# Kernel optimization log

Hardware: AMD Instinct MI355X
Metric: run time of the kernel (lower is better)

Reference implementation:

```python
import jax, jax.numpy as jnp
import numpy as np

N_HEAD = 12
NEG_INF = -1e30


def setup_inputs() -> dict:
    key = jax.random.key(0)
    ks = jax.random.split(key, 12)
    bs, q_len, c_len, d = 2, 2048, 2048, 768
    s = 1.0 / np.sqrt(d)
    return {
        "query": jax.random.normal(ks[0], (bs, q_len, d), jnp.float32),
        "context": jax.random.normal(ks[1], (bs, c_len, d), jnp.float32),
        "c_mask": jax.random.randint(ks[2], (bs, c_len), 0, 2, jnp.int32),
        "Wq_w": jax.random.normal(ks[3], (d, d), jnp.float32) * s,
        "Wq_b": jnp.zeros((d,), jnp.float32),
        "Wk_w": jax.random.normal(ks[4], (d, d), jnp.float32) * s,
        "Wk_b": jnp.zeros((d,), jnp.float32),
        "Wv_w": jax.random.normal(ks[5], (d, d), jnp.float32) * s,
        "Wv_b": jnp.zeros((d,), jnp.float32),
        "fc_w": jax.random.normal(ks[6], (d, d), jnp.float32) * s,
        "fc_b": jnp.zeros((d,), jnp.float32),
    }


def reference(query, context, c_mask, Wq_w, Wq_b, Wk_w, Wk_b, Wv_w, Wv_b, fc_w, fc_b):
    bs, q_len, d = query.shape
    c_len = context.shape[1]
    d_k = d // N_HEAD
    a = 1.0 / np.sqrt(d_k)

    # QKV projections (torch Linear: y = x @ W.T + b), split into heads
    q = (query @ Wq_w.T + Wq_b).reshape(bs, q_len, N_HEAD, d_k)
    k = (context @ Wk_w.T + Wk_b).reshape(bs, c_len, N_HEAD, d_k)
    v = (context @ Wv_w.T + Wv_b).reshape(bs, c_len, N_HEAD, d_k)

    # scores [bs, n_head, q_len, c_len]
    s = jnp.einsum('bqhd,bchd->bhqc', q, k) * a

    # mask_logits: s * m + (1 - m) * -1e30, mask broadcast over heads and q
    m = c_mask.astype(s.dtype)[:, None, None, :]
    s = s * m + (1.0 - m) * NEG_INF

    p = jax.nn.softmax(s, axis=-1)  # dropout p=0.0 -> identity

    out = jnp.einsum('bhqc,bchd->bqhd', p, v).reshape(bs, q_len, d)
    return out @ fc_w.T + fc_b
```

## Files before the change

kernel.cpp:

```cpp
#include <hip/hip_runtime.h>
#include <cstdint>

#define D_MODEL 768
#define NH      12
#define DKH     64
#define SEQ     2048
#define BS      2
#define MROWS   (BS*SEQ)

typedef __bf16 bf16x8 __attribute__((ext_vector_type(8)));
typedef float  f32x4  __attribute__((ext_vector_type(4)));
typedef unsigned int u32_as1 __attribute__((address_space(1)));
typedef unsigned int u32_as3 __attribute__((address_space(3)));

__device__ __forceinline__ void gld16(const void* g, void* l) {
  __builtin_amdgcn_global_load_lds((const u32_as1*)g, (u32_as3*)l, 16, 0, 0);
}
__device__ __forceinline__ unsigned short f2bf(float x) {
  return __builtin_bit_cast(unsigned short, (__bf16)x);
}

__global__ void cvt_all(
    const float* __restrict__ q, const float* __restrict__ c,
    const float* __restrict__ wq, const float* __restrict__ wk,
    const float* __restrict__ wv, const float* __restrict__ wf,
    unsigned short* __restrict__ oq, unsigned short* __restrict__ oc,
    unsigned short* __restrict__ owq, unsigned short* __restrict__ owk,
    unsigned short* __restrict__ owv, unsigned short* __restrict__ owf)
{
  const int b = blockIdx.x;
  const float* in; unsigned short* out; int i;
  if (b < 6144) {
    in = (b < 3072) ? q : c;
    out = (b < 3072) ? oq : oc;
    i = ((b < 3072) ? b : b - 3072) * 256 + threadIdx.x;
  } else {
    int wb = b - 6144, wi = wb / 576;
    in  = (wi == 0) ? wq : (wi == 1) ? wk : (wi == 2) ? wv : wf;
    out = (wi == 0) ? owq : (wi == 1) ? owk : (wi == 2) ? owv : owf;
    i = (wb - wi * 576) * 256 + threadIdx.x;
  }
  float4 v = reinterpret_cast<const float4*>(in)[i];
  ushort4 o; o.x = f2bf(v.x); o.y = f2bf(v.y); o.z = f2bf(v.z); o.w = f2bf(v.w);
  reinterpret_cast<ushort4*>(out)[i] = o;
}

__global__ void mask_bf(const int* __restrict__ m, unsigned short* __restrict__ o) {
  int i = blockIdx.x * 256 + threadIdx.x;
  o[i] = f2bf(m[i] ? 1.0f : 0.0f);
}

template<bool OUT_F32>
__device__ __forceinline__ void gemm64x128_body(
    const unsigned short* __restrict__ A, const unsigned short* __restrict__ B,
    const float* __restrict__ bias, int biasRow, void* __restrict__ Cout,
    int ldc, int m0, int n0, float outScale, const int* __restrict__ colMask)
{
  __shared__ alignas(16) char sA[2][8192];
  __shared__ alignas(16) char sB[2][16384];
  const int tid = threadIdx.x;
  const int w = tid >> 6, l = tid & 63;
  const int g16 = l >> 4, c16 = l & 15;
  const int wr = (w >> 1) * 32, wc = (w & 1) * 64;

  auto stageA = [&](int kt, char* dst) {
#pragma unroll
    for (int i = 0; i < 2; i++) {
      int ch = w * 2 + i;
      int X = ch * 1024 + l * 16;
      int row = X >> 7;
      int sl = ((X >> 4) & 7) ^ (row & 7);
      gld16(A + (size_t)(m0 + row) * 768 + kt + sl * 8, dst + ch * 1024);
    }
  };
  auto stageB = [&](int kt, char* dst) {
#pragma unroll
    for (int i = 0; i < 4; i++) {
      int ch = w * 4 + i;
      int X = ch * 1024 + l * 16;
      int row = X >> 7;
      int sl = ((X >> 4) & 7) ^ (row & 7);
      gld16(B + (size_t)(n0 + row) * 768 + kt + sl * 8, dst + ch * 1024);
    }
  };

  f32x4 acc[2][4];
#pragma unroll
  for (int m = 0; m < 2; m++)
#pragma unroll
    for (int n = 0; n < 4; n++) acc[m][n] = f32x4{0.f, 0.f, 0.f, 0.f};

  stageA(0, sA[0]);
  stageB(0, sB[0]);
  __syncthreads();
  int cur = 0;
  for (int kt = 0; kt < 768; kt += 64) {
    if (kt + 64 < 768) {
      stageA(kt + 64, sA[cur ^ 1]);
      stageB(kt + 64, sB[cur ^ 1]);
    }
    __builtin_amdgcn_s_setprio(1);
#pragma unroll
    for (int kk = 0; kk < 2; kk++) {
      bf16x8 af[2], bq[4];
#pragma unroll
      for (int m = 0; m < 2; m++) {
        int row = wr + m * 16 + c16, slot = kk * 4 + g16;
        af[m] = *(const bf16x8*)(sA[cur] + row * 128 + ((slot ^ (row & 7)) << 4));
      }
#pragma unroll
      for (int n = 0; n < 4; n++) {
        int row = wc + n * 16 + c16, slot = kk * 4 + g16;
        bq[n] = *(const bf16x8*)(sB[cur] + row * 128 + ((slot ^ (row & 7)) << 4));
      }
#pragma unroll
      for (int m = 0; m < 2; m++)
#pragma unroll
        for (int n = 0; n < 4; n++)
          acc[m][n] = __builtin_amdgcn_mfma_f32_16x16x32_bf16(af[m], bq[n], acc[m][n], 0, 0, 0);
    }
    __builtin_amdgcn_s_setprio(0);
    __syncthreads();
    cur ^= 1;
  }

#pragma unroll
  for (int m = 0; m < 2; m++)
#pragma unroll
    for (int n = 0; n < 4; n++)
#pragma unroll
      for (int r = 0; r < 4; r++) {
        int row = m0 + wr + m * 16 + g16 * 4 + r;
        int col = n0 + wc + n * 16 + c16;
        float v = (acc[m][n][r] + (biasRow ? bias[row] : bias[col])) * outScale;
        if (colMask) v *= (float)colMask[col];
        if constexpr (OUT_F32) ((float*)Cout)[(size_t)row * ldc + col] = v;
        else ((unsigned short*)Cout)[(size_t)row * ldc + col] = f2bf(v);
      }
}

#define QSCALE 0.1803368801111f

__global__ __launch_bounds__(256, 2) void gemm_qkv(
    const unsigned short* __restrict__ q_bf, const unsigned short* __restrict__ c_bf,
    const unsigned short* __restrict__ wq, const unsigned short* __restrict__ wk,
    const unsigned short* __restrict__ wv,
    const float* __restrict__ bq, const float* __restrict__ bk,
    const float* __restrict__ bv, const int* __restrict__ cmask,
    unsigned short* __restrict__ Qb, unsigned short* __restrict__ Kb,
    unsigned short* __restrict__ Vtb)
{
  const int x = blockIdx.x;
  const int lin = (x & 7) * 48 + (x >> 3);
  if (blockIdx.y == 0) {
    gemm64x128_body<false>(q_bf, wq, bq, 0, Qb, 768, (lin / 6) * 64, (lin % 6) * 128,
                           QSCALE, nullptr);
  } else if (blockIdx.y == 1) {
    gemm64x128_body<false>(c_bf, wk, bk, 0, Kb, 768, (lin / 6) * 64, (lin % 6) * 128,
                           1.0f, nullptr);
  } else {
    gemm64x128_body<false>(wv, c_bf, bv, 1, Vtb, 4096, (lin % 12) * 64, (lin / 12) * 128,
                           1.0f, cmask);
  }
}

__global__ __launch_bounds__(256, 4) void gemm_fc64(
    const unsigned short* __restrict__ A, const unsigned short* __restrict__ B,
    const float* __restrict__ bias, float* __restrict__ Cout)
{
  __shared__ alignas(16) char sA[2][8192];
  __shared__ alignas(16) char sB[2][8192];
  const int tid = threadIdx.x;
  const int w = tid >> 6, l = tid & 63;
  const int g16 = l >> 4, c16 = l & 15;
  const int flat = blockIdx.x;
  const int lin = (flat & 7) * 96 + (flat >> 3);
  const int tf = lin % 12, ts = lin / 12;
  const int m0 = ts * 64, n0 = tf * 64;
  const int wr = (w >> 1) * 32, wc = (w & 1) * 32;

  auto stage = [&](const unsigned short* __restrict__ P, int p0, int kt, char* dst) {
#pragma unroll
    for (int i = 0; i < 2; i++) {
      int ch = w * 2 + i;
      int X = ch * 1024 + l * 16;
      int row = X >> 7;
      int sl = ((X >> 4) & 7) ^ (row & 7);
      gld16(P + (size_t)(p0 + row) * 768 + kt + sl * 8, dst + ch * 1024);
    }
  };

  f32x4 acc[2][2];
#pragma unroll
  for (int m = 0; m < 2; m++)
#pragma unroll
    for (int n = 0; n < 2; n++) acc[m][n] = f32x4{0.f, 0.f, 0.f, 0.f};

  stage(A, m0, 0, sA[0]);
  stage(B, n0, 0, sB[0]);
  __syncthreads();
  int cur = 0;
  for (int kt = 0; kt < 768; kt += 64) {
    if (kt + 64 < 768) {
      stage(A, m0, kt + 64, sA[cur ^ 1]);
      stage(B, n0, kt + 64, sB[cur ^ 1]);
    }
    __builtin_amdgcn_s_setprio(1);
#pragma unroll
    for (int kk = 0; kk < 2; kk++) {
      bf16x8 af[2], bq[2];
#pragma unroll
      for (int m = 0; m < 2; m++) {
        int row = wr + m * 16 + c16, slot = kk * 4 + g16;
        af[m] = *(const bf16x8*)(sA[cur] + row * 128 + ((slot ^ (row & 7)) << 4));
      }
#pragma unroll
      for (int n = 0; n < 2; n++) {
        int row = wc + n * 16 + c16, slot = kk * 4 + g16;
        bq[n] = *(const bf16x8*)(sB[cur] + row * 128 + ((slot ^ (row & 7)) << 4));
      }
#pragma unroll
      for (int m = 0; m < 2; m++)
#pragma unroll
        for (int n = 0; n < 2; n++)
          acc[m][n] = __builtin_amdgcn_mfma_f32_16x16x32_bf16(af[m], bq[n], acc[m][n], 0, 0, 0);
    }
    __builtin_amdgcn_s_setprio(0);
    __syncthreads();
    cur ^= 1;
  }

#pragma unroll
  for (int m = 0; m < 2; m++)
#pragma unroll
    for (int n = 0; n < 2; n++)
#pragma unroll
      for (int r = 0; r < 4; r++) {
        int row = m0 + wr + m * 16 + g16 * 4 + r;
        int col = n0 + wc + n * 16 + c16;
        Cout[(size_t)row * 768 + col] = acc[m][n][r] + bias[col];
      }
}

__global__ __launch_bounds__(256, 4) void attn_kernel(
    const unsigned short* __restrict__ Qb, const unsigned short* __restrict__ Kb,
    const unsigned short* __restrict__ Vt, const unsigned short* __restrict__ maskbf,
    unsigned short* __restrict__ Ob)
{
  __shared__ alignas(16) char sK[2][8192];
  __shared__ alignas(16) char sV[2][8192];
  __shared__ alignas(16) char sP[8192];
  const int tid = threadIdx.x, w = tid >> 6, l = tid & 63;
  const int g16 = l >> 4, c16 = l & 15;
  const int flat = blockIdx.x;
  const int xcd = flat & 7, sidx = flat >> 3;
  const int p = xcd + 8 * (sidx >> 5);
  const int qt = sidx & 31;
  const int h = p % 12, b = p / 12;
  const int qrow0 = b * SEQ + qt * 64;
  const int crow0 = b * SEQ;

  bf16x8 qa[2];
  {
    const unsigned short* qp =
        Qb + (size_t)(qrow0 + w * 16 + c16) * D_MODEL + h * DKH + g16 * 8;
    qa[0] = *(const bf16x8*)(qp);
    qa[1] = *(const bf16x8*)(qp + 32);
  }

  auto stageK = [&](int ct, int buf) {
#pragma unroll
    for (int i = 0; i < 2; i++) {
      int ch = w * 2 + i;
      int X = ch * 1024 + l * 16;
      int row = X >> 7;
      int sl = ((X >> 4) & 7) ^ (row & 7);
      gld16(Kb + (size_t)(crow0 + ct + row) * D_MODEL + h * DKH + sl * 8,
            sK[buf] + ch * 1024);
    }
  };
  auto stageV = [&](int ct, int buf) {
#pragma unroll
    for (int i = 0; i < 2; i++) {
      int ch = w * 2 + i;
      int X = ch * 1024 + l * 16;
      int row = X >> 7;
      int sl = ((X >> 4) & 7) ^ (row & 7);
      gld16(Vt + (size_t)(h * DKH + row) * (size_t)MROWS + crow0 + ct + sl * 8,
            sV[buf] + ch * 1024);
    }
  };

  f32x4 accO[4], accL;
#pragma unroll
  for (int n = 0; n < 4; n++) accO[n] = f32x4{0.f, 0.f, 0.f, 0.f};
  accL = f32x4{0.f, 0.f, 0.f, 0.f};

  stageK(0, 0); stageV(0, 0);
  __syncthreads();
  int cur = 0;

  for (int ct = 0; ct < SEQ; ct += 64) {
    if (ct + 64 < SEQ) { stageK(ct + 64, cur ^ 1); stageV(ct + 64, cur ^ 1); }

    bf16x8 mfrag[2];
#pragma unroll
    for (int kk = 0; kk < 2; kk++)
      mfrag[kk] = *(const bf16x8*)(maskbf + crow0 + ct + kk * 32 + g16 * 8);

    f32x4 s[4];
#pragma unroll
    for (int n = 0; n < 4; n++) s[n] = f32x4{0.f, 0.f, 0.f, 0.f};
    __builtin_amdgcn_s_setprio(1);
#pragma unroll
    for (int kk = 0; kk < 2; kk++) {
      bf16x8 kf[4];
#pragma unroll
      for (int n = 0; n < 4; n++) {
        int row = n * 16 + c16, slot = kk * 4 + g16;
        kf[n] = *(const bf16x8*)(sK[cur] + row * 128 + ((slot ^ (row & 7)) << 4));
      }
#pragma unroll
      for (int n = 0; n < 4; n++)
        s[n] = __builtin_amdgcn_mfma_f32_16x16x32_bf16(qa[kk], kf[n], s[n], 0, 0, 0);
    }
    __builtin_amdgcn_s_setprio(0);

#pragma unroll
    for (int r = 0; r < 4; r++) {
      int prow = g16 * 4 + r;
#pragma unroll
      for (int n = 0; n < 4; n++) {
        float pv = __builtin_amdgcn_exp2f(s[n][r]);
        int slot = n * 2 + (c16 >> 3);
        int addr = w * 2048 + prow * 128 + ((slot ^ (prow & 7)) << 4) + (c16 & 7) * 2;
        *(__bf16*)(sP + addr) = (__bf16)pv;
      }
    }

    __builtin_amdgcn_s_setprio(1);
#pragma unroll
    for (int kk = 0; kk < 2; kk++) {
      bf16x8 pa, vf[4];
      {
        int prow = c16, slot = kk * 4 + g16;
        pa = *(const bf16x8*)(sP + w * 2048 + prow * 128 + ((slot ^ (prow & 7)) << 4));
      }
#pragma unroll
      for (int n = 0; n < 4; n++) {
        int vrow = n * 16 + c16, slot = kk * 4 + g16;
        vf[n] = *(const bf16x8*)(sV[cur] + vrow * 128 + ((slot ^ (vrow & 7)) << 4));
      }
#pragma unroll
      for (int n = 0; n < 4; n++)
        accO[n] = __builtin_amdgcn_mfma_f32_16x16x32_bf16(pa, vf[n], accO[n], 0, 0, 0);
      accL = __builtin_amdgcn_mfma_f32_16x16x32_bf16(pa, mfrag[kk], accL, 0, 0, 0);
    }
    __builtin_amdgcn_s_setprio(0);

    __syncthreads();
    cur ^= 1;
  }

#pragma unroll
  for (int r = 0; r < 4; r++) {
    float inv = 1.0f / accL[r];
#pragma unroll
    for (int n = 0; n < 4; n++) {
      int row = qrow0 + w * 16 + g16 * 4 + r;
      int col = h * DKH + n * 16 + c16;
      Ob[(size_t)row * D_MODEL + col] = f2bf(accO[n][r] * inv);
    }
  }
}

extern "C" void kernel_launch(void* const* d_in, const int* in_sizes, int n_in,
                              void* d_out, int out_size, void* d_ws, size_t ws_size,
                              hipStream_t stream) {
  const float* query   = (const float*)d_in[0];
  const float* context = (const float*)d_in[1];
  const int*   cmask   = (const int*)d_in[2];
  const float* Wq_w = (const float*)d_in[3];
  const float* Wq_b = (const float*)d_in[4];
  const float* Wk_w = (const float*)d_in[5];
  const float* Wk_b = (const float*)d_in[6];
  const float* Wv_w = (const float*)d_in[7];
  const float* Wv_b = (const float*)d_in[8];
  const float* fc_w = (const float*)d_in[9];
  const float* fc_b = (const float*)d_in[10];
  float* out = (float*)d_out;

  unsigned short* ws   = (unsigned short*)d_ws;
  const size_t NQ = (size_t)MROWS * D_MODEL;
  const size_t NW = (size_t)D_MODEL * D_MODEL;
  unsigned short* q_bf = ws;
  unsigned short* c_bf = q_bf + NQ;
  unsigned short* Qb   = c_bf + NQ;
  unsigned short* Kb   = Qb + NQ;
  unsigned short* Vtb  = Kb + NQ;
  unsigned short* Ob   = Vtb + NQ;
  unsigned short* wq   = Ob + NQ;
  unsigned short* wk   = wq + NW;
  unsigned short* wv   = wk + NW;
  unsigned short* wf   = wv + NW;
  unsigned short* maskbf = q_bf;

  cvt_all<<<8448, 256, 0, stream>>>(query, context, Wq_w, Wk_w, Wv_w, fc_w,
                                    q_bf, c_bf, wq, wk, wv, wf);

  gemm_qkv<<<dim3(384, 3), 256, 0, stream>>>(
      q_bf, c_bf, wq, wk, wv, Wq_b, Wk_b, Wv_b, cmask, Qb, Kb, Vtb);

  mask_bf<<<MROWS / 256, 256, 0, stream>>>(cmask, maskbf);

  attn_kernel<<<768, 256, 0, stream>>>(Qb, Kb, Vtb, maskbf, Ob);

  gemm_fc64<<<768, 256, 0, stream>>>(Ob, wf, fc_b, out);
}
```

Baseline: 96.23 us.

## Use two-wave attention blocks with 32 query rows per wave

The attention kernel now runs with 128 threads (2 waves) per block instead of 4, and each wave handles two 16-row query fragments. Each K and V fragment read from LDS is reused across two MFMA row tiles, which halves LDS reads per MFMA and doubles the staging work each wave issues. The cost is higher register pressure from doubled accumulators, and fewer waves per block to hide latency.

```diff
diff --git a/kernel.cpp b/kernel.cpp
--- a/kernel.cpp
+++ b/kernel.cpp
@@ -242,7 +242,7 @@
       }
 }
 
-__global__ __launch_bounds__(256, 4) void attn_kernel(
+__global__ __launch_bounds__(128, 2) void attn_kernel(
     const unsigned short* __restrict__ Qb, const unsigned short* __restrict__ Kb,
     const unsigned short* __restrict__ Vt, const unsigned short* __restrict__ maskbf,
     unsigned short* __restrict__ Ob)
@@ -260,18 +260,19 @@
   const int qrow0 = b * SEQ + qt * 64;
   const int crow0 = b * SEQ;
 
-  bf16x8 qa[2];
-  {
+  bf16x8 qa[2][2];
+#pragma unroll
+  for (int m = 0; m < 2; m++) {
     const unsigned short* qp =
-        Qb + (size_t)(qrow0 + w * 16 + c16) * D_MODEL + h * DKH + g16 * 8;
-    qa[0] = *(const bf16x8*)(qp);
-    qa[1] = *(const bf16x8*)(qp + 32);
+        Qb + (size_t)(qrow0 + w * 32 + m * 16 + c16) * D_MODEL + h * DKH + g16 * 8;
+    qa[m][0] = *(const bf16x8*)(qp);
+    qa[m][1] = *(const bf16x8*)(qp + 32);
   }
 
   auto stageK = [&](int ct, int buf) {
 #pragma unroll
-    for (int i = 0; i < 2; i++) {
-      int ch = w * 2 + i;
+    for (int i = 0; i < 4; i++) {
+      int ch = w * 4 + i;
       int X = ch * 1024 + l * 16;
       int row = X >> 7;
       int sl = ((X >> 4) & 7) ^ (row & 7);
@@ -281,8 +282,8 @@
   };
   auto stageV = [&](int ct, int buf) {
 #pragma unroll
-    for (int i = 0; i < 2; i++) {
-      int ch = w * 2 + i;
+    for (int i = 0; i < 4; i++) {
+      int ch = w * 4 + i;
       int X = ch * 1024 + l * 16;
       int row = X >> 7;
       int sl = ((X >> 4) & 7) ^ (row & 7);
@@ -291,10 +292,13 @@
     }
   };
 
-  f32x4 accO[4], accL;
-#pragma unroll
-  for (int n = 0; n < 4; n++) accO[n] = f32x4{0.f, 0.f, 0.f, 0.f};
-  accL = f32x4{0.f, 0.f, 0.f, 0.f};
+  f32x4 accO[2][4], accL[2];
+#pragma unroll
+  for (int m = 0; m < 2; m++) {
+#pragma unroll
+    for (int n = 0; n < 4; n++) accO[m][n] = f32x4{0.f, 0.f, 0.f, 0.f};
+    accL[m] = f32x4{0.f, 0.f, 0.f, 0.f};
+  }
 
   stageK(0, 0); stageV(0, 0);
   __syncthreads();
@@ -308,9 +312,11 @@
     for (int kk = 0; kk < 2; kk++)
       mfrag[kk] = *(const bf16x8*)(maskbf + crow0 + ct + kk * 32 + g16 * 8);
 
-    f32x4 s[4];
-#pragma unroll
-    for (int n = 0; n < 4; n++) s[n] = f32x4{0.f, 0.f, 0.f, 0.f};
+    f32x4 s[2][4];
+#pragma unroll
+    for (int m = 0; m < 2; m++)
+#pragma unroll
+      for (int n = 0; n < 4; n++) s[m][n] = f32x4{0.f, 0.f, 0.f, 0.f};
     __builtin_amdgcn_s_setprio(1);
 #pragma unroll
     for (int kk = 0; kk < 2; kk++) {
@@ -321,30 +327,35 @@
         kf[n] = *(const bf16x8*)(sK[cur] + row * 128 + ((slot ^ (row & 7)) << 4));
       }
 #pragma unroll
-      for (int n = 0; n < 4; n++)
-        s[n] = __builtin_amdgcn_mfma_f32_16x16x32_bf16(qa[kk], kf[n], s[n], 0, 0, 0);
+      for (int m = 0; m < 2; m++)
+#pragma unroll
+        for (int n = 0; n < 4; n++)
+          s[m][n] = __builtin_amdgcn_mfma_f32_16x16x32_bf16(qa[m][kk], kf[n], s[m][n], 0, 0, 0);
     }
     __builtin_amdgcn_s_setprio(0);
 
 #pragma unroll
-    for (int r = 0; r < 4; r++) {
-      int prow = g16 * 4 + r;
-#pragma unroll
-      for (int n = 0; n < 4; n++) {
-        float pv = __builtin_amdgcn_exp2f(s[n][r]);
-        int slot = n * 2 + (c16 >> 3);
-        int addr = w * 2048 + prow * 128 + ((slot ^ (prow & 7)) << 4) + (c16 & 7) * 2;
-        *(__bf16*)(sP + addr) = (__bf16)pv;
-      }
-    }
+    for (int m = 0; m < 2; m++)
+#pragma unroll
+      for (int r = 0; r < 4; r++) {
+        int prow = m * 16 + g16 * 4 + r;
+#pragma unroll
+        for (int n = 0; n < 4; n++) {
+          float pv = __builtin_amdgcn_exp2f(s[m][n][r]);
+          int slot = n * 2 + (c16 >> 3);
+          int addr = w * 4096 + prow * 128 + ((slot ^ (prow & 7)) << 4) + (c16 & 7) * 2;
+          *(__bf16*)(sP + addr) = (__bf16)pv;
+        }
+      }
 
     __builtin_amdgcn_s_setprio(1);
 #pragma unroll
     for (int kk = 0; kk < 2; kk++) {
-      bf16x8 pa, vf[4];
-      {
-        int prow = c16, slot = kk * 4 + g16;
-        pa = *(const bf16x8*)(sP + w * 2048 + prow * 128 + ((slot ^ (prow & 7)) << 4));
+      bf16x8 pa[2], vf[4];
+#pragma unroll
+      for (int m = 0; m < 2; m++) {
+        int prow = m * 16 + c16, slot = kk * 4 + g16;
+        pa[m] = *(const bf16x8*)(sP + w * 4096 + prow * 128 + ((slot ^ (prow & 7)) << 4));
       }
 #pragma unroll
       for (int n = 0; n < 4; n++) {
@@ -352,9 +363,12 @@
         vf[n] = *(const bf16x8*)(sV[cur] + vrow * 128 + ((slot ^ (vrow & 7)) << 4));
       }
 #pragma unroll
-      for (int n = 0; n < 4; n++)
-        accO[n] = __builtin_amdgcn_mfma_f32_16x16x32_bf16(pa, vf[n], accO[n], 0, 0, 0);
-      accL = __builtin_amdgcn_mfma_f32_16x16x32_bf16(pa, mfrag[kk], accL, 0, 0, 0);
+      for (int m = 0; m < 2; m++) {
+#pragma unroll
+        for (int n = 0; n < 4; n++)
+          accO[m][n] = __builtin_amdgcn_mfma_f32_16x16x32_bf16(pa[m], vf[n], accO[m][n], 0, 0, 0);
+        accL[m] = __builtin_amdgcn_mfma_f32_16x16x32_bf16(pa[m], mfrag[kk], accL[m], 0, 0, 0);
+      }
     }
     __builtin_amdgcn_s_setprio(0);
 
@@ -363,15 +377,17 @@
   }
 
 #pragma unroll
-  for (int r = 0; r < 4; r++) {
-    float inv = 1.0f / accL[r];
-#pragma unroll
-    for (int n = 0; n < 4; n++) {
-      int row = qrow0 + w * 16 + g16 * 4 + r;
-      int col = h * DKH + n * 16 + c16;
-      Ob[(size_t)row * D_MODEL + col] = f2bf(accO[n][r] * inv);
-    }
-  }
+  for (int m = 0; m < 2; m++)
+#pragma unroll
+    for (int r = 0; r < 4; r++) {
+      float inv = 1.0f / accL[m][r];
+#pragma unroll
+      for (int n = 0; n < 4; n++) {
+        int row = qrow0 + w * 32 + m * 16 + g16 * 4 + r;
+        int col = h * DKH + n * 16 + c16;
+        Ob[(size_t)row * D_MODEL + col] = f2bf(accO[m][n][r] * inv);
+      }
+    }
 }
 
 extern "C" void kernel_launch(void* const* d_in, const int* in_sizes, int n_in,
@@ -413,7 +429,7 @@
 
   mask_bf<<<MROWS / 256, 256, 0, stream>>>(cmask, maskbf);
 
-  attn_kernel<<<768, 256, 0, stream>>>(Qb, Kb, Vtb, maskbf, Ob);
+  attn_kernel<<<768, 128, 0, stream>>>(Qb, Kb, Vtb, maskbf, Ob);
 
   gemm_fc64<<<768, 256, 0, stream>>>(Ob, wf, fc_b, out);
 }
```

Result: slower. 101.1 us (+5.0%).

## Keep attention probabilities in registers by computing transposed scores

Applied to the files above, without the earlier changes.

Swaps the MFMA operand order for the QK^T product so the score accumulator comes out transposed, which lets each lane build the P operand for the PV MFMA directly from its own exp2 results. This removes the shared-memory round trip for P (the scalar bf16 stores, the read-back and the sP buffer). To match the new k-index mapping, the V fragments and mask fragments are now assembled from two 4-element loads each. The trade is more, narrower LDS and global loads for V and the mask, but fewer LDS bytes, less LDS capacity per block and no store-then-load dependency.

```diff
diff --git a/kernel.cpp b/kernel.cpp
--- a/kernel.cpp
+++ b/kernel.cpp
@@ -9,6 +9,7 @@
 #define MROWS   (BS*SEQ)
 
 typedef __bf16 bf16x8 __attribute__((ext_vector_type(8)));
+typedef __bf16 bf16x4 __attribute__((ext_vector_type(4)));
 typedef float  f32x4  __attribute__((ext_vector_type(4)));
 typedef unsigned int u32_as1 __attribute__((address_space(1)));
 typedef unsigned int u32_as3 __attribute__((address_space(3)));
@@ -249,7 +250,6 @@
 {
   __shared__ alignas(16) char sK[2][8192];
   __shared__ alignas(16) char sV[2][8192];
-  __shared__ alignas(16) char sP[8192];
   const int tid = threadIdx.x, w = tid >> 6, l = tid & 63;
   const int g16 = l >> 4, c16 = l & 15;
   const int flat = blockIdx.x;
@@ -259,6 +259,7 @@
   const int h = p % 12, b = p / 12;
   const int qrow0 = b * SEQ + qt * 64;
   const int crow0 = b * SEQ;
+  const int gLow = g16 >> 1, gOddB = (g16 & 1) * 8;
 
   bf16x8 qa[2];
   {
@@ -305,12 +306,16 @@
 
     bf16x8 mfrag[2];
 #pragma unroll
-    for (int kk = 0; kk < 2; kk++)
-      mfrag[kk] = *(const bf16x8*)(maskbf + crow0 + ct + kk * 32 + g16 * 8);
-
-    f32x4 s[4];
-#pragma unroll
-    for (int n = 0; n < 4; n++) s[n] = f32x4{0.f, 0.f, 0.f, 0.f};
+    for (int kk = 0; kk < 2; kk++) {
+      const unsigned short* mp = maskbf + crow0 + ct + kk * 32 + g16 * 4;
+      bf16x4 m0 = *(const bf16x4*)(mp);
+      bf16x4 m1 = *(const bf16x4*)(mp + 16);
+      mfrag[kk] = __builtin_shufflevector(m0, m1, 0, 1, 2, 3, 4, 5, 6, 7);
+    }
+
+    f32x4 s4[4];
+#pragma unroll
+    for (int n = 0; n < 4; n++) s4[n] = f32x4{0.f, 0.f, 0.f, 0.f};
     __builtin_amdgcn_s_setprio(1);
 #pragma unroll
     for (int kk = 0; kk < 2; kk++) {
@@ -322,39 +327,33 @@
       }
 #pragma unroll
       for (int n = 0; n < 4; n++)
-        s[n] = __builtin_amdgcn_mfma_f32_16x16x32_bf16(qa[kk], kf[n], s[n], 0, 0, 0);
+        s4[n] = __builtin_amdgcn_mfma_f32_16x16x32_bf16(kf[n], qa[kk], s4[n], 0, 0, 0);
     }
     __builtin_amdgcn_s_setprio(0);
 
-#pragma unroll
-    for (int r = 0; r < 4; r++) {
-      int prow = g16 * 4 + r;
+    bf16x8 paf[2];
+#pragma unroll
+    for (int kk = 0; kk < 2; kk++)
+#pragma unroll
+      for (int j = 0; j < 4; j++) {
+        paf[kk][j]     = (__bf16)__builtin_amdgcn_exp2f(s4[2 * kk][j]);
+        paf[kk][j + 4] = (__bf16)__builtin_amdgcn_exp2f(s4[2 * kk + 1][j]);
+      }
+
+    __builtin_amdgcn_s_setprio(1);
+#pragma unroll
+    for (int kk = 0; kk < 2; kk++) {
 #pragma unroll
       for (int n = 0; n < 4; n++) {
-        float pv = __builtin_amdgcn_exp2f(s[n][r]);
-        int slot = n * 2 + (c16 >> 3);
-        int addr = w * 2048 + prow * 128 + ((slot ^ (prow & 7)) << 4) + (c16 & 7) * 2;
-        *(__bf16*)(sP + addr) = (__bf16)pv;
-      }
-    }
-
-    __builtin_amdgcn_s_setprio(1);
-#pragma unroll
-    for (int kk = 0; kk < 2; kk++) {
-      bf16x8 pa, vf[4];
-      {
-        int prow = c16, slot = kk * 4 + g16;
-        pa = *(const bf16x8*)(sP + w * 2048 + prow * 128 + ((slot ^ (prow & 7)) << 4));
-      }
-#pragma unroll
-      for (int n = 0; n < 4; n++) {
-        int vrow = n * 16 + c16, slot = kk * 4 + g16;
-        vf[n] = *(const bf16x8*)(sV[cur] + vrow * 128 + ((slot ^ (vrow & 7)) << 4));
-      }
-#pragma unroll
-      for (int n = 0; n < 4; n++)
-        accO[n] = __builtin_amdgcn_mfma_f32_16x16x32_bf16(pa, vf[n], accO[n], 0, 0, 0);
-      accL = __builtin_amdgcn_mfma_f32_16x16x32_bf16(pa, mfrag[kk], accL, 0, 0, 0);
+        int row = n * 16 + c16;
+        const char* base = sV[cur] + row * 128 + gOddB;
+        int s1 = kk * 4 + gLow, s2 = s1 + 2;
+        bf16x4 v0 = *(const bf16x4*)(base + ((s1 ^ (row & 7)) << 4));
+        bf16x4 v1 = *(const bf16x4*)(base + ((s2 ^ (row & 7)) << 4));
+        bf16x8 vf = __builtin_shufflevector(v0, v1, 0, 1, 2, 3, 4, 5, 6, 7);
+        accO[n] = __builtin_amdgcn_mfma_f32_16x16x32_bf16(paf[kk], vf, accO[n], 0, 0, 0);
+      }
+      accL = __builtin_amdgcn_mfma_f32_16x16x32_bf16(paf[kk], mfrag[kk], accL, 0, 0, 0);
     }
     __builtin_amdgcn_s_setprio(0);
 
```

Result: faster. 94.08 us (-2.2%).
